# Optimization experiments

Measured on AMD Instinct MI355X. Metric: run time of the kernel, lower is better.

Reference implementation:

```python
import jax, jax.numpy as jnp
import numpy as np

B, N, DS, DP, H, DH, DFF = 1, 1024, 768, 128, 16, 48, 1536


def _ln(x, eps=1e-5):
    m = jnp.mean(x, axis=-1, keepdims=True)
    v = jnp.var(x, axis=-1, keepdims=True)
    return (x - m) * jax.lax.rsqrt(v + eps)


def _ada_ln(a, s, gw, gb, bw):
    # AF3-style adaptive layernorm: sigmoid(Linear(LN(s))) * LN(a) + Linear(LN(s))
    sn = _ln(s)
    return jax.nn.sigmoid(sn @ gw + gb) * _ln(a) + sn @ bw


def setup_inputs() -> dict:
    key = jax.random.key(0)
    ks = jax.random.split(key, 24)
    w = lambda k, shape: jax.random.normal(k, shape, dtype=jnp.float32) * 0.02
    return {
        'x': jax.random.normal(ks[0], (B, N, DS), dtype=jnp.float32),
        'single_cond': jax.random.normal(ks[1], (B, N, DS), dtype=jnp.float32),
        'pair_cond': jax.random.normal(ks[2], (B, N, N, DP), dtype=jnp.float32),
        'attn_gamma_w': w(ks[3], (DS, DS)), 'attn_gamma_b': jnp.zeros((DS,), jnp.float32),
        'attn_beta_w': w(ks[4], (DS, DS)),
        'wq': w(ks[5], (DS, H * DH)), 'bq': jnp.zeros((H * DH,), jnp.float32),
        'wk': w(ks[6], (DS, H * DH)), 'wv': w(ks[7], (DS, H * DH)),
        'wb': w(ks[8], (DP, H)),
        'wg': w(ks[9], (DS, H * DH)),
        'wo': w(ks[10], (H * DH, DS)),
        'attn_gate_w': w(ks[11], (DS, DS)), 'attn_gate_b': jnp.full((DS,), -2.0, jnp.float32),
        'ff_gamma_w': w(ks[12], (DS, DS)), 'ff_gamma_b': jnp.zeros((DS,), jnp.float32),
        'ff_beta_w': w(ks[13], (DS, DS)),
        'ff_w1': w(ks[14], (DS, DFF)), 'ff_w2': w(ks[15], (DS, DFF)),
        'ff_w3': w(ks[16], (DFF, DS)),
        'ff_gate_w': w(ks[17], (DS, DS)), 'ff_gate_b': jnp.full((DS,), -2.0, jnp.float32),
        'mask': jnp.ones((B, N), dtype=bool),
    }


def reference(x, single_cond, pair_cond, attn_gamma_w, attn_gamma_b, attn_beta_w,
              wq, bq, wk, wv, wb, wg, wo, attn_gate_w, attn_gate_b,
              ff_gamma_w, ff_gamma_b, ff_beta_w, ff_w1, ff_w2, ff_w3,
              ff_gate_w, ff_gate_b, mask):
    # --- AttentionPairBias (edge bias + cond adaLN + gated output) ---
    a = _ada_ln(x, single_cond, attn_gamma_w, attn_gamma_b, attn_beta_w)
    q = (a @ wq + bq).reshape(B, N, H, DH)  # q has bias (q_use_bias=True)
    k = (a @ wk).reshape(B, N, H, DH)
    v = (a @ wv).reshape(B, N, H, DH)
    bias = jnp.einsum('bijp,ph->bhij', _ln(pair_cond), wb)  # pair bias per head
    logits = jnp.einsum('bihd,bjhd->bhij', q, k) * (1.0 / np.float32(np.sqrt(DH))) + bias
    logits = jnp.where(mask[:, None, None, :], logits, jnp.float32(-1e9))
    attn = jax.nn.softmax(logits, axis=-1)
    o = jnp.einsum('bhij,bjhd->bihd', attn, v)
    g = jax.nn.sigmoid(a @ wg).reshape(B, N, H, DH)  # gating (g_use_bias=False)
    attn_out = (g * o).reshape(B, N, H * DH) @ wo  # o_use_bias=False
    attn_out = jax.nn.sigmoid(single_cond @ attn_gate_w + attn_gate_b) * attn_out
    # --- ConditionedFeedForward (adaLN + SwiGLU + cond output gate) ---
    f = _ada_ln(x, single_cond, ff_gamma_w, ff_gamma_b, ff_beta_w)
    h = jax.nn.silu(f @ ff_w1) * (f @ ff_w2)
    ff_out = jax.nn.sigmoid(single_cond @ ff_gate_w + ff_gate_b) * (h @ ff_w3)
    # dropout p=0 (eval) -> identity; residual add of both branches
    return x + attn_out + ff_out
```

## Files before the change

### kernel.cpp

```cpp
#include <hip/hip_runtime.h>
#include <hip/hip_bf16.h>


typedef __attribute__((ext_vector_type(8))) short bf16x8;
typedef __attribute__((ext_vector_type(4))) float f32x4;
typedef __attribute__((ext_vector_type(4))) unsigned short us4;

#define DEVFN static __device__ __forceinline__

DEVFN float bf2f(unsigned short u){
  union { unsigned int u; float f; } v; v.u = ((unsigned int)u) << 16; return v.f;
}
DEVFN unsigned short f2bf(float f){
  union { float f; unsigned int u; } v; v.f = f;
  unsigned int r = v.u + 0x7fffu + ((v.u >> 16) & 1u);
  return (unsigned short)(r >> 16);
}
DEVFN float sigf(float x){ return 1.f / (1.f + __expf(-x)); }

DEVFN void gload16(const void* g, void* l){
  __builtin_amdgcn_global_load_lds(
      (const __attribute__((address_space(1))) void*)g,
      (__attribute__((address_space(3))) void*)l, 16, 0, 0);
}

#define OFF_SN    0x0000000ULL
#define OFF_SC    0x0180000ULL
#define OFF_XA    0x0300000ULL
#define OFF_W1    0x0600000ULL
#define OFF_W2    0x0A80000ULL
#define OFF_W3    0x0CC0000ULL
#define OFF_W4    0x1140000ULL
#define OFF_W5    0x15C0000ULL
#define OFF_W6    0x1800000ULL
#define OFF_BIAS1 0x1920000ULL
#define OFF_BIASG 0x1923000ULL
#define OFF_BIASQ 0x1924800ULL
#define OFF_G1    0x1930000ULL
#define OFF_GATES 0x2530000ULL
#define OFF_A     0x2B30000ULL
#define OFF_F     0x2CB0000ULL
#define OFF_QH    0x2E30000ULL
#define OFF_KH    0x2FB0000ULL
#define OFF_GH    0x3130000ULL
#define OFF_VT    0x3430000ULL
#define OFF_HH    0x4030000ULL
#define OFF_GO    0x4330000ULL
#define OFF_PB    0x47B0000ULL

struct WJobs {
  const float* src[14];
  unsigned long long dst[14];
  int K[14];
  int N[14];
  int rowmul[14];
  int rowoff[14];
};

__global__ __launch_bounds__(256) void prep_kernel(WJobs jobs, char* ws,
    const float* __restrict__ x, const float* __restrict__ sc,
    unsigned short* __restrict__ sn_bf, unsigned short* __restrict__ sc_bf,
    float* __restrict__ xa,
    const float* agb, const float* bq, const float* gtb, const float* fgtb,
    const float* fgb, float* bias1, float* biasg, float* biasq){
  const int bid = blockIdx.x;
  const int tid = threadIdx.x;
  if(bid < 9792){
    int t = bid, z = 0;
    while(true){
      int nt = (jobs.N[z] >> 5) * (jobs.K[z] >> 5);
      if(t < nt) break;
      t -= nt; z++;
    }
    const int nx = jobs.N[z] >> 5;
    const int n0 = (t % nx) << 5, k0 = (t / nx) << 5;
    const int K = jobs.K[z], N = jobs.N[z];
    __shared__ float tt[32][33];
    const int tx = tid & 31, ty = tid >> 5;
    const float* src = jobs.src[z];
    #pragma unroll
    for(int i=0;i<4;i++)
      tt[ty + i*8][tx] = src[(long long)(k0 + ty + i*8) * N + n0 + tx];
    __syncthreads();
    unsigned short* dst = (unsigned short*)(ws + jobs.dst[z]);
    const int rm = jobs.rowmul[z], ro = jobs.rowoff[z];
    #pragma unroll
    for(int i=0;i<4;i++)
      dst[(long long)((n0 + ty + i*8)*rm + ro) * K + k0 + tx] = f2bf(tt[tx][ty + i*8]);
    return;
  }
  if(bid >= 10816){
    int t = (bid - 10816) * 256 + tid;
    float v = 0.f;
    if(t < 768) v = agb[t];
    else if(t >= 1536 && t < 2304) v = fgb[t - 1536];
    bias1[t] = v;
    biasq[t] = (t < 768) ? bq[t] : 0.f;
    if(t < 1536) biasg[t] = (t < 768) ? gtb[t] : fgtb[t - 768];
    return;
  }
  const int row = bid - 9792;
  const float* xr = x + (long long)row * 768;
  const float* sr = sc + (long long)row * 768;
  float xs[3], ss[3];
  float s0=0.f, s1=0.f, s2=0.f, s3=0.f;
  #pragma unroll
  for(int i=0;i<3;i++){
    float xv = xr[tid + i*256], sv = sr[tid + i*256];
    xs[i]=xv; ss[i]=sv;
    s0 += xv; s1 += xv*xv; s2 += sv; s3 += sv*sv;
  }
  #pragma unroll
  for(int o=32;o;o>>=1){
    s0 += __shfl_xor(s0,o); s1 += __shfl_xor(s1,o);
    s2 += __shfl_xor(s2,o); s3 += __shfl_xor(s3,o);
  }
  __shared__ float red[4][4];
  const int w = tid >> 6;
  if((tid & 63) == 0){ red[0][w]=s0; red[1][w]=s1; red[2][w]=s2; red[3][w]=s3; }
  __syncthreads();
  float tx0 = red[0][0]+red[0][1]+red[0][2]+red[0][3];
  float tx1 = red[1][0]+red[1][1]+red[1][2]+red[1][3];
  float ts0 = red[2][0]+red[2][1]+red[2][2]+red[2][3];
  float ts1 = red[3][0]+red[3][1]+red[3][2]+red[3][3];
  const float inv = 1.f/768.f;
  float mx = tx0*inv, vx = tx1*inv - mx*mx;
  float ms = ts0*inv, vs = ts1*inv - ms*ms;
  float rsx = rsqrtf(vx + 1e-5f), rss = rsqrtf(vs + 1e-5f);
  #pragma unroll
  for(int i=0;i<3;i++){
    int c = tid + i*256;
    xa[(long long)row*768 + c]    = (xs[i]-mx)*rsx;
    sn_bf[(long long)row*768 + c] = f2bf((ss[i]-ms)*rss);
    sc_bf[(long long)row*768 + c] = f2bf(ss[i]);
  }
}

DEVFN void gemm_tile_f32(const unsigned short* __restrict__ A,
                         const unsigned short* __restrict__ Bt,
                         int N, int K, int m0, int n0,
                         const float* __restrict__ bias,
                         float* __restrict__ Cf, int epi,
                         unsigned short* sA, unsigned short* sB, int tid){
  const int w = tid >> 6, l = tid & 63, l15 = l & 15, l4 = l >> 4;
  const int wm = w >> 1, wn = w & 1;
  f32x4 zf = {0.f,0.f,0.f,0.f};
  f32x4 acc[4][4];
  #pragma unroll
  for(int m=0;m<4;m++)
    #pragma unroll
    for(int n=0;n<4;n++) acc[m][n] = zf;

  const int srow = w*16 + (l >> 2);
  const int scol = (l & 3) * 8;
  const unsigned short* gA = A  + (long long)(m0 + srow) * K + scol;
  const unsigned short* gB = Bt + (long long)(n0 + srow) * K + scol;
  unsigned short* lA0 = &sA[(w*16)*32];
  unsigned short* lA1 = &sA[(64 + w*16)*32];
  unsigned short* lB0 = &sB[(w*16)*32];
  unsigned short* lB1 = &sB[(64 + w*16)*32];
  const long long half = (long long)64 * K;

  for(int k0 = 0; k0 < K; k0 += 32){
    gload16(gA + k0, lA0);
    gload16(gA + half + k0, lA1);
    gload16(gB + k0, lB0);
    gload16(gB + half + k0, lB1);
    __syncthreads();
    bf16x8 af[4], bg[4];
    #pragma unroll
    for(int m=0;m<4;m++) af[m] = *(const bf16x8*)&sA[(wm*64 + m*16 + l15)*32 + l4*8];
    #pragma unroll
    for(int n=0;n<4;n++) bg[n] = *(const bf16x8*)&sB[(wn*64 + n*16 + l15)*32 + l4*8];
    #pragma unroll
    for(int m=0;m<4;m++)
      #pragma unroll
      for(int n=0;n<4;n++)
        acc[m][n] = __builtin_amdgcn_mfma_f32_16x16x32_bf16(af[m], bg[n], acc[m][n], 0, 0, 0);
    __syncthreads();
  }
  #pragma unroll
  for(int m=0;m<4;m++){
    #pragma unroll
    for(int n=0;n<4;n++){
      #pragma unroll
      for(int r=0;r<4;r++){
        const int i = m0 + wm*64 + m*16 + l4*4 + r;
        const int c = n0 + wn*64 + n*16 + l15;
        float v = acc[m][n][r] + bias[c];
        Cf[(long long)i*N + c] = epi ? sigf(v) : v;
      }
    }
  }
}

DEVFN void pair_block(int pbid, const float* __restrict__ pair,
                      const float* __restrict__ wb,
                      unsigned short* __restrict__ pb, int tid){
  const int l = tid & 63, w = tid >> 6, l15 = l & 15, l4 = l >> 4;
  bf16x8 wbf[4];
  #pragma unroll
  for(int c=0;c<4;c++){
    bf16x8 t;
    #pragma unroll
    for(int e=0;e<8;e++) t[e] = (short)f2bf(wb[(c*32 + l4*8 + e)*16 + l15]);
    wbf[c] = t;
  }
  f32x4 zf = {0.f,0.f,0.f,0.f};
  #pragma unroll
  for(int q=0;q<4;q++){
    const long long tile = (long long)pbid * 16 + q*4 + w;
    const long long row0 = tile << 4;
    const float* pr = pair + ((row0 + l15) << 7);
    float vals[32];
    #pragma unroll
    for(int c=0;c<4;c++){
      float4 v0 = *(const float4*)(pr + c*32 + l4*8);
      float4 v1 = *(const float4*)(pr + c*32 + l4*8 + 4);
      vals[c*8+0]=v0.x; vals[c*8+1]=v0.y; vals[c*8+2]=v0.z; vals[c*8+3]=v0.w;
      vals[c*8+4]=v1.x; vals[c*8+5]=v1.y; vals[c*8+6]=v1.z; vals[c*8+7]=v1.w;
    }
    float s=0.f, s2=0.f;
    #pragma unroll
    for(int e=0;e<32;e++){ s += vals[e]; s2 += vals[e]*vals[e]; }
    s += __shfl_xor(s, 16); s2 += __shfl_xor(s2, 16);
    s += __shfl_xor(s, 32); s2 += __shfl_xor(s2, 32);
    const float m = s * (1.f/128.f);
    const float rs = rsqrtf(s2*(1.f/128.f) - m*m + 1e-5f);
    f32x4 acc = zf;
    #pragma unroll
    for(int c=0;c<4;c++){
      bf16x8 af;
      #pragma unroll
      for(int e=0;e<8;e++) af[e] = (short)f2bf((vals[c*8+e] - m) * rs);
      acc = __builtin_amdgcn_mfma_f32_16x16x32_bf16(af, wbf[c], acc, 0,0,0);
    }
    us4 o;
    #pragma unroll
    for(int r=0;r<4;r++) o[r] = f2bf(acc[r]);
    *(us4*)&pb[((long long)l15 << 20) + row0 + l4*4] = o;
  }
}

__global__ __launch_bounds__(256) void fA_kernel(
    const float* __restrict__ pair, const float* __restrict__ wb,
    unsigned short* __restrict__ pb,
    const unsigned short* __restrict__ SN, const unsigned short* __restrict__ W1,
    const float* __restrict__ B1, float* __restrict__ G1,
    const unsigned short* __restrict__ SC, const unsigned short* __restrict__ W2,
    const float* __restrict__ BG, float* __restrict__ GT){
  __shared__ __align__(16) unsigned short sA[128*32];
  __shared__ __align__(16) unsigned short sB[128*32];
  const int bid = blockIdx.x;
  const int tid = threadIdx.x;
  if(bid < 288){
    if(bid < 192){
      gemm_tile_f32(SN, W1, 3072, 768, (bid & 7)*128, (bid >> 3)*128, B1, G1, 0, sA, sB, tid);
    } else {
      const int t = bid - 192;
      gemm_tile_f32(SC, W2, 1536, 768, (t & 7)*128, (t >> 3)*128, BG, GT, 1, sA, sB, tid);
    }
    return;
  }
  pair_block(bid - 288, pair, wb, pb, tid);
}

__global__ __launch_bounds__(256) void ew1_kernel(const float* __restrict__ g1,
    const float* __restrict__ xa, unsigned short* __restrict__ a_bf,
    unsigned short* __restrict__ f_bf, const float* __restrict__ x,
    float* __restrict__ out){
  const int i = blockIdx.x;
  const int c = blockIdx.y * 256 + threadIdx.x;
  const float* row = g1 + (long long)i * 3072;
  float xv = xa[(long long)i*768 + c];
  a_bf[(long long)i*768 + c] = f2bf(sigf(row[c])      * xv + row[768 + c]);
  f_bf[(long long)i*768 + c] = f2bf(sigf(row[1536+c]) * xv + row[2304 + c]);
  out[(long long)i*768 + c] = x[(long long)i*768 + c];
}

__global__ __launch_bounds__(256) void fB_kernel(
    const float* __restrict__ pair, const float* __restrict__ wb,
    unsigned short* __restrict__ pb,
    const unsigned short* __restrict__ A_, const unsigned short* __restrict__ W3,
    const float* __restrict__ BQ,
    unsigned short* __restrict__ QH, unsigned short* __restrict__ KH,
    unsigned short* __restrict__ GH, unsigned short* __restrict__ VT,
    const unsigned short* __restrict__ F_, const unsigned short* __restrict__ W4,
    unsigned short* __restrict__ HH){
  __shared__ __align__(16) unsigned short sA[128*32];
  __shared__ __align__(16) unsigned short sB[128*32];
  const int bid = blockIdx.x;
  const int tid = threadIdx.x;
  if(bid >= 384){
    pair_block(bid - 384 + 2048, pair, wb, pb, tid);
    return;
  }
  const bool isq = bid < 192;
  const int t = isq ? bid : bid - 192;
  const int m0 = (t & 7) * 128, n0 = (t >> 3) * 128;
  const unsigned short* A  = isq ? A_ : F_;
  const unsigned short* Bt = isq ? W3 : W4;
  const int K = 768;

  const int w = tid >> 6, l = tid & 63, l15 = l & 15, l4 = l >> 4;
  const int wm = w >> 1, wn = w & 1;
  f32x4 zf = {0.f,0.f,0.f,0.f};
  f32x4 acc[4][4];
  #pragma unroll
  for(int m=0;m<4;m++)
    #pragma unroll
    for(int n=0;n<4;n++) acc[m][n] = zf;

  const int srow = w*16 + (l >> 2);
  const int scol = (l & 3) * 8;
  const unsigned short* gA = A  + (long long)(m0 + srow) * K + scol;
  const unsigned short* gB = Bt + (long long)(n0 + srow) * K + scol;
  unsigned short* lA0 = &sA[(w*16)*32];
  unsigned short* lA1 = &sA[(64 + w*16)*32];
  unsigned short* lB0 = &sB[(w*16)*32];
  unsigned short* lB1 = &sB[(64 + w*16)*32];
  const long long half = (long long)64 * K;

  for(int k0 = 0; k0 < K; k0 += 32){
    gload16(gA + k0, lA0);
    gload16(gA + half + k0, lA1);
    gload16(gB + k0, lB0);
    gload16(gB + half + k0, lB1);
    __syncthreads();
    bf16x8 af[4], bg[4];
    #pragma unroll
    for(int m=0;m<4;m++) af[m] = *(const bf16x8*)&sA[(wm*64 + m*16 + l15)*32 + l4*8];
    #pragma unroll
    for(int n=0;n<4;n++) bg[n] = *(const bf16x8*)&sB[(wn*64 + n*16 + l15)*32 + l4*8];
    #pragma unroll
    for(int m=0;m<4;m++)
      #pragma unroll
      for(int n=0;n<4;n++)
        acc[m][n] = __builtin_amdgcn_mfma_f32_16x16x32_bf16(af[m], bg[n], acc[m][n], 0, 0, 0);
    __syncthreads();
  }
  if(isq){
    #pragma unroll
    for(int m=0;m<4;m++){
      #pragma unroll
      for(int n=0;n<4;n++){
        const int c = n0 + wn*64 + n*16 + l15;
        const int ibase = m0 + wm*64 + m*16 + l4*4;
        const int which = c / 768;
        const int h = (c % 768) / 48, d = c % 48;
        unsigned short vb[4];
        #pragma unroll
        for(int r=0;r<4;r++) vb[r] = f2bf(acc[m][n][r] + BQ[c]);
        if(which == 2){
          us4 o; o.x=vb[0]; o.y=vb[1]; o.z=vb[2]; o.w=vb[3];
          *(us4*)&VT[((long long)(c - 1536) << 10) + ibase] = o;
        } else {
          unsigned short* dst = (which == 0) ? QH : (which == 1) ? KH : GH;
          #pragma unroll
          for(int r=0;r<4;r++)
            dst[((long long)((h << 10) + ibase + r))*48 + d] = vb[r];
        }
      }
    }
  } else {
    #pragma unroll
    for(int m=0;m<4;m++){
      #pragma unroll
      for(int n=0;n<4;n++){
        #pragma unroll
        for(int r=0;r<4;r++){
          const int i = m0 + wm*64 + m*16 + l4*4 + r;
          const int c = n0 + wn*64 + n*16 + l15;
          float v = acc[m][n][r];
          float partner = __shfl_xor(v, 1);
          if((c & 1) == 0)
            HH[(long long)i*1536 + (c>>1)] = f2bf(v * sigf(v) * partner);
        }
      }
    }
  }
}

__global__ __launch_bounds__(256) void attn_kernel(
    const unsigned short* __restrict__ QH, const unsigned short* __restrict__ KH,
    const unsigned short* __restrict__ GH,
    const unsigned short* __restrict__ pbias,
    const unsigned short* __restrict__ VT,
    unsigned short* __restrict__ go){
  const int h  = blockIdx.x >> 6;
  const int i0 = (blockIdx.x & 63) << 4;
  const int tid = threadIdx.x;
  const int w = tid >> 6, l = tid & 63, l15 = l & 15, l4 = l >> 4;

  __shared__ unsigned short sP[16][1032];
  __shared__ float sRedM[16][4];
  __shared__ float sRedS[16][4];
  __shared__ float sO[4][16][48];

  f32x4 zf = {0.f,0.f,0.f,0.f};
  bf16x8 zero8 = {0,0,0,0,0,0,0,0};

  const unsigned short* pbh = pbias + ((long long)h << 20) + ((long long)i0 << 10);
  #pragma unroll
  for(int it=0; it<8; it++){
    const int idx = it*2048 + tid*8;
    const int r = idx >> 10, c = idx & 1023;
    *(bf16x8*)&sP[r][c] = *(const bf16x8*)&pbh[((long long)r << 10) + c];
  }

  f32x4 accs[16];
  #pragma unroll
  for(int f=0;f<16;f++) accs[f] = zf;
  bf16x8 aq0, aq1;
  {
    const unsigned short* qp = QH + (long long)((h << 10) + i0 + l15)*48;
    aq0 = *(const bf16x8*)(qp + l4*8);
    aq1 = *(const bf16x8*)(qp + 32 + l4*8);
  }
  const int jbase = w * 256;
  #pragma unroll
  for(int f=0; f<16; f++){
    const int j = jbase + f*16 + l15;
    const unsigned short* kp = KH + (long long)((h << 10) + j)*48;
    bf16x8 bk0 = *(const bf16x8*)(kp + l4*8);
    bf16x8 bk1 = *(const bf16x8*)(kp + 32 + l4*8);
    if(l4 >= 2) bk1 = zero8;
    accs[f] = __builtin_amdgcn_mfma_f32_16x16x32_bf16(aq0, bk0, accs[f], 0,0,0);
    accs[f] = __builtin_amdgcn_mfma_f32_16x16x32_bf16(aq1, bk1, accs[f], 0,0,0);
  }
  __syncthreads();

  const float scale = 0.14433756729740643f;
  #pragma unroll
  for(int f=0;f<16;f++){
    #pragma unroll
    for(int r=0;r<4;r++)
      accs[f][r] = accs[f][r]*scale + bf2f(sP[l4*4 + r][jbase + f*16 + l15]);
  }
  float pm[4];
  #pragma unroll
  for(int r=0;r<4;r++){
    float m = accs[0][r];
    #pragma unroll
    for(int f=1;f<16;f++) m = fmaxf(m, accs[f][r]);
    #pragma unroll
    for(int o=1;o<16;o<<=1) m = fmaxf(m, __shfl_xor(m, o));
    pm[r] = m;
  }
  if(l15 == 0){
    #pragma unroll
    for(int r=0;r<4;r++) sRedM[l4*4 + r][w] = pm[r];
  }
  __syncthreads();
  float rowm[4];
  #pragma unroll
  for(int r=0;r<4;r++){
    const int i = l4*4 + r;
    rowm[r] = fmaxf(fmaxf(sRedM[i][0], sRedM[i][1]), fmaxf(sRedM[i][2], sRedM[i][3]));
  }
  float psum[4] = {0.f,0.f,0.f,0.f};
  #pragma unroll
  for(int f=0;f<16;f++)
    #pragma unroll
    for(int r=0;r<4;r++){
      float p = __expf(accs[f][r] - rowm[r]);
      accs[f][r] = p;
      psum[r] += p;
    }
  #pragma unroll
  for(int r=0;r<4;r++)
    #pragma unroll
    for(int o=1;o<16;o<<=1) psum[r] += __shfl_xor(psum[r], o);
  if(l15 == 0){
    #pragma unroll
    for(int r=0;r<4;r++) sRedS[l4*4 + r][w] = psum[r];
  }
  #pragma unroll
  for(int f=0;f<16;f++)
    #pragma unroll
    for(int r=0;r<4;r++)
      sP[l4*4 + r][jbase + f*16 + l15] = f2bf(accs[f][r]);

  f32x4 acco[3];
  #pragma unroll
  for(int n=0;n<3;n++) acco[n] = zf;
  const unsigned short* vth = VT + ((long long)(h*48) << 10);
  #pragma unroll
  for(int c=0; c<4; c++){
    const int jb = jbase + c*64;
    #pragma unroll
    for(int kk=0; kk<2; kk++){
      bf16x8 pa = *(const bf16x8*)&sP[l15][jb + kk*32 + l4*8];
      #pragma unroll
      for(int n=0;n<3;n++){
        bf16x8 bv = *(const bf16x8*)&vth[((long long)(n*16 + l15) << 10) + jb + kk*32 + l4*8];
        acco[n] = __builtin_amdgcn_mfma_f32_16x16x32_bf16(pa, bv, acco[n], 0,0,0);
      }
    }
  }
  #pragma unroll
  for(int n=0;n<3;n++)
    #pragma unroll
    for(int r=0;r<4;r++)
      sO[w][l4*4 + r][n*16 + l15] = acco[n][r];
  __syncthreads();
  for(int t = tid; t < 768; t += 256){
    const int i = t / 48, d = t % 48;
    float o = sO[0][i][d] + sO[1][i][d] + sO[2][i][d] + sO[3][i][d];
    float lsum = sRedS[i][0] + sRedS[i][1] + sRedS[i][2] + sRedS[i][3];
    float gv = bf2f(GH[(long long)((h << 10) + i0 + i)*48 + d]);
    go[(long long)(i0 + i)*768 + h*48 + d] = f2bf(sigf(gv) * (o / lsum));
  }
}

__global__ __launch_bounds__(256) void final_kernel(
    const unsigned short* __restrict__ GO, const unsigned short* __restrict__ W6t,
    const unsigned short* __restrict__ HH, const unsigned short* __restrict__ W5t,
    const float* __restrict__ gates, float* __restrict__ out){
  __shared__ __align__(16) unsigned short sA[128*32];
  __shared__ __align__(16) unsigned short sB[128*32];
  const int m0 = blockIdx.x * 128, n0 = blockIdx.y * 128;
  const int z = blockIdx.z;
  const bool pA = z < 4;
  const unsigned short* A  = pA ? GO  : HH;
  const unsigned short* Bt = pA ? W6t : W5t;
  const int K    = pA ? 768 : 1536;
  const int kbeg = pA ? z*192 : (z-4)*384;
  const int kend = pA ? kbeg + 192 : kbeg + 384;
  const int goff = pA ? 0 : 768;
  const int tid = threadIdx.x;
  const int w = tid >> 6, l = tid & 63, l15 = l & 15, l4 = l >> 4;
  const int wm = w >> 1, wn = w & 1;
  f32x4 zf = {0.f,0.f,0.f,0.f};
  f32x4 acc[4][4];
  #pragma unroll
  for(int m=0;m<4;m++)
    #pragma unroll
    for(int n=0;n<4;n++) acc[m][n] = zf;

  const int srow = w*16 + (l >> 2);
  const int scol = (l & 3) * 8;
  const unsigned short* gA = A  + (long long)(m0 + srow) * K + scol;
  const unsigned short* gB = Bt + (long long)(n0 + srow) * K + scol;
  unsigned short* lA0 = &sA[(w*16)*32];
  unsigned short* lA1 = &sA[(64 + w*16)*32];
  unsigned short* lB0 = &sB[(w*16)*32];
  unsigned short* lB1 = &sB[(64 + w*16)*32];
  const long long half = (long long)64 * K;

  for(int k0 = kbeg; k0 < kend; k0 += 32){
    gload16(gA + k0, lA0);
    gload16(gA + half + k0, lA1);
    gload16(gB + k0, lB0);
    gload16(gB + half + k0, lB1);
    __syncthreads();
    bf16x8 af[4], bg[4];
    #pragma unroll
    for(int m=0;m<4;m++) af[m] = *(const bf16x8*)&sA[(wm*64 + m*16 + l15)*32 + l4*8];
    #pragma unroll
    for(int n=0;n<4;n++) bg[n] = *(const bf16x8*)&sB[(wn*64 + n*16 + l15)*32 + l4*8];
    #pragma unroll
    for(int m=0;m<4;m++)
      #pragma unroll
      for(int n=0;n<4;n++)
        acc[m][n] = __builtin_amdgcn_mfma_f32_16x16x32_bf16(af[m], bg[n], acc[m][n], 0, 0, 0);
    __syncthreads();
  }
  #pragma unroll
  for(int m=0;m<4;m++){
    #pragma unroll
    for(int n=0;n<4;n++){
      #pragma unroll
      for(int r=0;r<4;r++){
        const int i = m0 + wm*64 + m*16 + l4*4 + r;
        const int c = n0 + wn*64 + n*16 + l15;
        float v = gates[(long long)i*1536 + goff + c] * acc[m][n][r];
        __hip_atomic_fetch_add(&out[(long long)i*768 + c], v,
                               __ATOMIC_RELAXED, __HIP_MEMORY_SCOPE_AGENT);
      }
    }
  }
}

extern "C" void kernel_launch(void* const* d_in, const int* in_sizes, int n_in,
                              void* d_out, int out_size, void* d_ws, size_t ws_size,
                              hipStream_t stream){
  (void)in_sizes; (void)n_in; (void)out_size; (void)ws_size;
  const float* x    = (const float*)d_in[0];
  const float* sc   = (const float*)d_in[1];
  const float* pair = (const float*)d_in[2];
  const float* agw  = (const float*)d_in[3];
  const float* agb  = (const float*)d_in[4];
  const float* abw  = (const float*)d_in[5];
  const float* wq   = (const float*)d_in[6];
  const float* bq   = (const float*)d_in[7];
  const float* wk   = (const float*)d_in[8];
  const float* wv   = (const float*)d_in[9];
  const float* wb   = (const float*)d_in[10];
  const float* wg   = (const float*)d_in[11];
  const float* wo   = (const float*)d_in[12];
  const float* gtw  = (const float*)d_in[13];
  const float* gtb  = (const float*)d_in[14];
  const float* fgw  = (const float*)d_in[15];
  const float* fgb  = (const float*)d_in[16];
  const float* fbw  = (const float*)d_in[17];
  const float* fw1  = (const float*)d_in[18];
  const float* fw2  = (const float*)d_in[19];
  const float* fw3  = (const float*)d_in[20];
  const float* fgtw = (const float*)d_in[21];
  const float* fgtb = (const float*)d_in[22];
  float* out = (float*)d_out;
  char* ws = (char*)d_ws;

  unsigned short* SN   = (unsigned short*)(ws + OFF_SN);
  unsigned short* SC   = (unsigned short*)(ws + OFF_SC);
  float*          XA   = (float*)(ws + OFF_XA);
  unsigned short* W1   = (unsigned short*)(ws + OFF_W1);
  unsigned short* W2   = (unsigned short*)(ws + OFF_W2);
  unsigned short* W3   = (unsigned short*)(ws + OFF_W3);
  unsigned short* W4   = (unsigned short*)(ws + OFF_W4);
  unsigned short* W5   = (unsigned short*)(ws + OFF_W5);
  unsigned short* W6   = (unsigned short*)(ws + OFF_W6);
  float*          B1   = (float*)(ws + OFF_BIAS1);
  float*          BG   = (float*)(ws + OFF_BIASG);
  float*          BQ   = (float*)(ws + OFF_BIASQ);
  float*          G1   = (float*)(ws + OFF_G1);
  float*          GT   = (float*)(ws + OFF_GATES);
  unsigned short* A_   = (unsigned short*)(ws + OFF_A);
  unsigned short* F_   = (unsigned short*)(ws + OFF_F);
  unsigned short* QH   = (unsigned short*)(ws + OFF_QH);
  unsigned short* KH   = (unsigned short*)(ws + OFF_KH);
  unsigned short* GH   = (unsigned short*)(ws + OFF_GH);
  unsigned short* VT   = (unsigned short*)(ws + OFF_VT);
  unsigned short* HH   = (unsigned short*)(ws + OFF_HH);
  unsigned short* GO   = (unsigned short*)(ws + OFF_GO);
  unsigned short* PB   = (unsigned short*)(ws + OFF_PB);

  WJobs jobs;
  int ji = 0;
  auto setj = [&](const float* s, unsigned long long off, int K, int N,
                  int rm = 1, int ro = 0){
    jobs.src[ji]=s; jobs.dst[ji]=off; jobs.K[ji]=K; jobs.N[ji]=N;
    jobs.rowmul[ji]=rm; jobs.rowoff[ji]=ro; ji++;
  };
  const unsigned long long W768 = 768ULL*768ULL*2ULL;
  setj(agw,  OFF_W1 + 0*W768, 768, 768);
  setj(abw,  OFF_W1 + 1*W768, 768, 768);
  setj(fgw,  OFF_W1 + 2*W768, 768, 768);
  setj(fbw,  OFF_W1 + 3*W768, 768, 768);
  setj(gtw,  OFF_W2 + 0*W768, 768, 768);
  setj(fgtw, OFF_W2 + 1*W768, 768, 768);
  setj(wq,   OFF_W3 + 0*W768, 768, 768);
  setj(wk,   OFF_W3 + 1*W768, 768, 768);
  setj(wv,   OFF_W3 + 2*W768, 768, 768);
  setj(wg,   OFF_W3 + 3*W768, 768, 768);
  setj(fw1,  OFF_W4, 768, 1536, 2, 0);
  setj(fw2,  OFF_W4, 768, 1536, 2, 1);
  setj(fw3,  OFF_W5, 1536, 768);
  setj(wo,   OFF_W6, 768, 768);

  prep_kernel<<<10828, 256, 0, stream>>>(jobs, ws, x, sc, SN, SC, XA,
      agb, bq, gtb, fgtb, fgb, B1, BG, BQ);
  fA_kernel<<<2336, 256, 0, stream>>>(pair, wb, PB, SN, W1, B1, G1, SC, W2, BG, GT);
  ew1_kernel<<<dim3(1024,3), 256, 0, stream>>>(G1, XA, A_, F_, x, out);
  fB_kernel<<<2432, 256, 0, stream>>>(pair, wb, PB, A_, W3, BQ,
      QH, KH, GH, VT, F_, W4, HH);
  attn_kernel<<<1024, 256, 0, stream>>>(QH, KH, GH, PB, VT, GO);
  final_kernel<<<dim3(8,6,8), 256, 0, stream>>>(GO, W6, HH, W5, GT, out);
}
```

Measured before the change: 265.9 us.

## Spread weight transposes across kernels and overlap FFN output GEMM with attention

Splits the weight-transpose jobs: only the adaLN/gate weights are converted in the prep kernel, and the remaining weights are transposed by extra blocks in fA_kernel alongside the pair-bias work. The FFN down-projection (HH·W5) slices are moved into the attention kernel as extra blocks, so they run concurrently with attention, and the final kernel handles only the Wo projection. The pair-layernorm bf16 conversion switches to truncation instead of round-to-nearest, which is cheaper but slightly less accurate. The aim is to shorten the serial critical path and fill idle CUs, at the cost of larger shared-memory footprints and mixed block types within a kernel.

Result: no change. 265.0 us (-0.3%).

```diff
diff --git a/kernel.cpp b/kernel.cpp
--- a/kernel.cpp
+++ b/kernel.cpp
@@ -15,6 +15,10 @@
   union { float f; unsigned int u; } v; v.f = f;
   unsigned int r = v.u + 0x7fffu + ((v.u >> 16) & 1u);
   return (unsigned short)(r >> 16);
+}
+DEVFN unsigned short f2bf_trunc(float f){
+  union { float f; unsigned int u; } v; v.f = f;
+  return (unsigned short)(v.u >> 16);
 }
 DEVFN float sigf(float x){ return 1.f / (1.f + __expf(-x)); }
 
@@ -49,48 +53,53 @@
 #define OFF_PB    0x47B0000ULL
 
 struct WJobs {
-  const float* src[14];
-  unsigned long long dst[14];
-  int K[14];
-  int N[14];
-  int rowmul[14];
-  int rowoff[14];
+  const float* src[8];
+  unsigned long long dst[8];
+  int K[8];
+  int N[8];
+  int rowmul[8];
+  int rowoff[8];
 };
 
-__global__ __launch_bounds__(256) void prep_kernel(WJobs jobs, char* ws,
+DEVFN void transpose_tile(const WJobs& jobs, char* ws, int t, int tid, void* smem){
+  int z = 0;
+  while(true){
+    int nt = (jobs.N[z] >> 5) * (jobs.K[z] >> 5);
+    if(t < nt) break;
+    t -= nt; z++;
+  }
+  const int nx = jobs.N[z] >> 5;
+  const int n0 = (t % nx) << 5, k0 = (t / nx) << 5;
+  const int K = jobs.K[z], N = jobs.N[z];
+  float (*tt)[33] = (float(*)[33])smem;
+  const int tx = tid & 31, ty = tid >> 5;
+  const float* src = jobs.src[z];
+  #pragma unroll
+  for(int i=0;i<4;i++)
+    tt[ty + i*8][tx] = src[(long long)(k0 + ty + i*8) * N + n0 + tx];
+  __syncthreads();
+  unsigned short* dst = (unsigned short*)(ws + jobs.dst[z]);
+  const int rm = jobs.rowmul[z], ro = jobs.rowoff[z];
+  #pragma unroll
+  for(int i=0;i<4;i++)
+    dst[(long long)((n0 + ty + i*8)*rm + ro) * K + k0 + tx] = f2bf(tt[tx][ty + i*8]);
+}
+
+__global__ __launch_bounds__(256) void prep_kernel(WJobs jobsP, char* ws,
     const float* __restrict__ x, const float* __restrict__ sc,
     unsigned short* __restrict__ sn_bf, unsigned short* __restrict__ sc_bf,
     float* __restrict__ xa,
     const float* agb, const float* bq, const float* gtb, const float* fgtb,
     const float* fgb, float* bias1, float* biasg, float* biasq){
+  __shared__ __align__(16) char smem[4352];
   const int bid = blockIdx.x;
   const int tid = threadIdx.x;
-  if(bid < 9792){
-    int t = bid, z = 0;
-    while(true){
-      int nt = (jobs.N[z] >> 5) * (jobs.K[z] >> 5);
-      if(t < nt) break;
-      t -= nt; z++;
-    }
-    const int nx = jobs.N[z] >> 5;
-    const int n0 = (t % nx) << 5, k0 = (t / nx) << 5;
-    const int K = jobs.K[z], N = jobs.N[z];
-    __shared__ float tt[32][33];
-    const int tx = tid & 31, ty = tid >> 5;
-    const float* src = jobs.src[z];
-    #pragma unroll
-    for(int i=0;i<4;i++)
-      tt[ty + i*8][tx] = src[(long long)(k0 + ty + i*8) * N + n0 + tx];
-    __syncthreads();
-    unsigned short* dst = (unsigned short*)(ws + jobs.dst[z]);
-    const int rm = jobs.rowmul[z], ro = jobs.rowoff[z];
-    #pragma unroll
-    for(int i=0;i<4;i++)
-      dst[(long long)((n0 + ty + i*8)*rm + ro) * K + k0 + tx] = f2bf(tt[tx][ty + i*8]);
+  if(bid < 3456){
+    transpose_tile(jobsP, ws, bid, tid, smem);
     return;
   }
-  if(bid >= 10816){
-    int t = (bid - 10816) * 256 + tid;
+  if(bid >= 4480){
+    int t = (bid - 4480) * 256 + tid;
     float v = 0.f;
     if(t < 768) v = agb[t];
     else if(t >= 1536 && t < 2304) v = fgb[t - 1536];
@@ -99,7 +108,7 @@
     if(t < 1536) biasg[t] = (t < 768) ? gtb[t] : fgtb[t - 768];
     return;
   }
-  const int row = bid - 9792;
+  const int row = bid - 3456;
   const float* xr = x + (long long)row * 768;
   const float* sr = sc + (long long)row * 768;
   float xs[3], ss[3];
@@ -115,7 +124,7 @@
     s0 += __shfl_xor(s0,o); s1 += __shfl_xor(s1,o);
     s2 += __shfl_xor(s2,o); s3 += __shfl_xor(s3,o);
   }
-  __shared__ float red[4][4];
+  float (*red)[4] = (float(*)[4])smem;
   const int w = tid >> 6;
   if((tid & 63) == 0){ red[0][w]=s0; red[1][w]=s1; red[2][w]=s2; red[3][w]=s3; }
   __syncthreads();
@@ -206,11 +215,9 @@
     for(int e=0;e<8;e++) t[e] = (short)f2bf(wb[(c*32 + l4*8 + e)*16 + l15]);
     wbf[c] = t;
   }
-  f32x4 zf = {0.f,0.f,0.f,0.f};
   #pragma unroll
   for(int q=0;q<4;q++){
-    const long long tile = (long long)pbid * 16 + q*4 + w;
-    const long long row0 = tile << 4;
+    const long long row0 = (((long long)pbid) * 16 + q*4 + w) << 4;
     const float* pr = pair + ((row0 + l15) << 7);
     float vals[32];
     #pragma unroll
@@ -227,12 +234,12 @@
     s += __shfl_xor(s, 32); s2 += __shfl_xor(s2, 32);
     const float m = s * (1.f/128.f);
     const float rs = rsqrtf(s2*(1.f/128.f) - m*m + 1e-5f);
-    f32x4 acc = zf;
+    f32x4 acc = {0.f,0.f,0.f,0.f};
     #pragma unroll
     for(int c=0;c<4;c++){
       bf16x8 af;
       #pragma unroll
-      for(int e=0;e<8;e++) af[e] = (short)f2bf((vals[c*8+e] - m) * rs);
+      for(int e=0;e<8;e++) af[e] = (short)f2bf_trunc((vals[c*8+e] - m) * rs);
       acc = __builtin_amdgcn_mfma_f32_16x16x32_bf16(af, wbf[c], acc, 0,0,0);
     }
     us4 o;
@@ -243,6 +250,7 @@
 }
 
 __global__ __launch_bounds__(256) void fA_kernel(
+    WJobs jobsA, char* ws,
     const float* __restrict__ pair, const float* __restrict__ wb,
     unsigned short* __restrict__ pb,
     const unsigned short* __restrict__ SN, const unsigned short* __restrict__ W1,
@@ -262,7 +270,11 @@
     }
     return;
   }
-  pair_block(bid - 288, pair, wb, pb, tid);
+  if(bid < 6624){
+    transpose_tile(jobsA, ws, bid - 288, tid, sA);
+    return;
+  }
+  pair_block(bid - 6624, pair, wb, pb, tid);
 }
 
 __global__ __launch_bounds__(256) void ew1_kernel(const float* __restrict__ g1,
@@ -381,29 +393,99 @@
   }
 }
 
+DEVFN void final_slice(const unsigned short* __restrict__ A,
+                       const unsigned short* __restrict__ Bt,
+                       int K, int kbeg, int kend, int goff, int m0, int n0,
+                       const float* __restrict__ gates, float* __restrict__ out,
+                       unsigned short* sA, unsigned short* sB, int tid){
+  const int w = tid >> 6, l = tid & 63, l15 = l & 15, l4 = l >> 4;
+  const int wm = w >> 1, wn = w & 1;
+  f32x4 zf = {0.f,0.f,0.f,0.f};
+  f32x4 acc[4][4];
+  #pragma unroll
+  for(int m=0;m<4;m++)
+    #pragma unroll
+    for(int n=0;n<4;n++) acc[m][n] = zf;
+
+  const int srow = w*16 + (l >> 2);
+  const int scol = (l & 3) * 8;
+  const unsigned short* gA = A  + (long long)(m0 + srow) * K + scol;
+  const unsigned short* gB = Bt + (long long)(n0 + srow) * K + scol;
+  unsigned short* lA0 = &sA[(w*16)*32];
+  unsigned short* lA1 = &sA[(64 + w*16)*32];
+  unsigned short* lB0 = &sB[(w*16)*32];
+  unsigned short* lB1 = &sB[(64 + w*16)*32];
+  const long long half = (long long)64 * K;
+
+  for(int k0 = kbeg; k0 < kend; k0 += 32){
+    gload16(gA + k0, lA0);
+    gload16(gA + half + k0, lA1);
+    gload16(gB + k0, lB0);
+    gload16(gB + half + k0, lB1);
+    __syncthreads();
+    bf16x8 af[4], bg[4];
+    #pragma unroll
+    for(int m=0;m<4;m++) af[m] = *(const bf16x8*)&sA[(wm*64 + m*16 + l15)*32 + l4*8];
+    #pragma unroll
+    for(int n=0;n<4;n++) bg[n] = *(const bf16x8*)&sB[(wn*64 + n*16 + l15)*32 + l4*8];
+    #pragma unroll
+    for(int m=0;m<4;m++)
+      #pragma unroll
+      for(int n=0;n<4;n++)
+        acc[m][n] = __builtin_amdgcn_mfma_f32_16x16x32_bf16(af[m], bg[n], acc[m][n], 0, 0, 0);
+    __syncthreads();
+  }
+  #pragma unroll
+  for(int m=0;m<4;m++){
+    #pragma unroll
+    for(int n=0;n<4;n++){
+      #pragma unroll
+      for(int r=0;r<4;r++){
+        const int i = m0 + wm*64 + m*16 + l4*4 + r;
+        const int c = n0 + wn*64 + n*16 + l15;
+        float v = gates[(long long)i*1536 + goff + c] * acc[m][n][r];
+        __hip_atomic_fetch_add(&out[(long long)i*768 + c], v,
+                               __ATOMIC_RELAXED, __HIP_MEMORY_SCOPE_AGENT);
+      }
+    }
+  }
+}
+
 __global__ __launch_bounds__(256) void attn_kernel(
     const unsigned short* __restrict__ QH, const unsigned short* __restrict__ KH,
     const unsigned short* __restrict__ GH,
     const unsigned short* __restrict__ pbias,
     const unsigned short* __restrict__ VT,
-    unsigned short* __restrict__ go){
-  const int h  = blockIdx.x >> 6;
-  const int i0 = (blockIdx.x & 63) << 4;
+    unsigned short* __restrict__ go,
+    const unsigned short* __restrict__ HH, const unsigned short* __restrict__ W5t,
+    const float* __restrict__ gates, float* __restrict__ out){
+  __shared__ __align__(16) char smem[45824];
+  const int bid = blockIdx.x;
   const int tid = threadIdx.x;
+  if(bid < 192){
+    const int z = bid / 48, rem = bid % 48;
+    final_slice(HH, W5t, 1536, z*384, z*384 + 384, 768,
+                (rem & 7)*128, (rem >> 3)*128, gates, out,
+                (unsigned short*)smem, (unsigned short*)(smem + 8192), tid);
+    return;
+  }
+  const int it = bid - 192;
+  const int h  = it >> 6;
+  const int i0 = (it & 63) << 4;
   const int w = tid >> 6, l = tid & 63, l15 = l & 15, l4 = l >> 4;
 
-  __shared__ unsigned short sP[16][1032];
-  __shared__ float sRedM[16][4];
-  __shared__ float sRedS[16][4];
-  __shared__ float sO[4][16][48];
+  unsigned short (*sP)[1032] = (unsigned short(*)[1032])smem;
+  float (*sRedM)[4] = (float(*)[4])(smem + 33024);
+  float (*sRedS)[4] = (float(*)[4])(smem + 33280);
+  float (*sO)[16][48] = (float(*)[16][48])(smem + 33536);
 
   f32x4 zf = {0.f,0.f,0.f,0.f};
   bf16x8 zero8 = {0,0,0,0,0,0,0,0};
 
   const unsigned short* pbh = pbias + ((long long)h << 20) + ((long long)i0 << 10);
   #pragma unroll
-  for(int it=0; it<8; it++){
-    const int idx = it*2048 + tid*8;
+  for(int itr=0; itr<8; itr++){
+    const int idx = itr*2048 + tid*8;
     const int r = idx >> 10, c = idx & 1023;
     *(bf16x8*)&sP[r][c] = *(const bf16x8*)&pbh[((long long)r << 10) + c];
   }
@@ -513,73 +595,13 @@
   }
 }
 
-__global__ __launch_bounds__(256) void final_kernel(
+__global__ __launch_bounds__(256) void finalA_kernel(
     const unsigned short* __restrict__ GO, const unsigned short* __restrict__ W6t,
-    const unsigned short* __restrict__ HH, const unsigned short* __restrict__ W5t,
     const float* __restrict__ gates, float* __restrict__ out){
   __shared__ __align__(16) unsigned short sA[128*32];
   __shared__ __align__(16) unsigned short sB[128*32];
-  const int m0 = blockIdx.x * 128, n0 = blockIdx.y * 128;
-  const int z = blockIdx.z;
-  const bool pA = z < 4;
-  const unsigned short* A  = pA ? GO  : HH;
-  const unsigned short* Bt = pA ? W6t : W5t;
-  const int K    = pA ? 768 : 1536;
-  const int kbeg = pA ? z*192 : (z-4)*384;
-  const int kend = pA ? kbeg + 192 : kbeg + 384;
-  const int goff = pA ? 0 : 768;
-  const int tid = threadIdx.x;
-  const int w = tid >> 6, l = tid & 63, l15 = l & 15, l4 = l >> 4;
-  const int wm = w >> 1, wn = w & 1;
-  f32x4 zf = {0.f,0.f,0.f,0.f};
-  f32x4 acc[4][4];
-  #pragma unroll
-  for(int m=0;m<4;m++)
-    #pragma unroll
-    for(int n=0;n<4;n++) acc[m][n] = zf;
-
-  const int srow = w*16 + (l >> 2);
-  const int scol = (l & 3) * 8;
-  const unsigned short* gA = A  + (long long)(m0 + srow) * K + scol;
-  const unsigned short* gB = Bt + (long long)(n0 + srow) * K + scol;
-  unsigned short* lA0 = &sA[(w*16)*32];
-  unsigned short* lA1 = &sA[(64 + w*16)*32];
-  unsigned short* lB0 = &sB[(w*16)*32];
-  unsigned short* lB1 = &sB[(64 + w*16)*32];
-  const long long half = (long long)64 * K;
-
-  for(int k0 = kbeg; k0 < kend; k0 += 32){
-    gload16(gA + k0, lA0);
-    gload16(gA + half + k0, lA1);
-    gload16(gB + k0, lB0);
-    gload16(gB + half + k0, lB1);
-    __syncthreads();
-    bf16x8 af[4], bg[4];
-    #pragma unroll
-    for(int m=0;m<4;m++) af[m] = *(const bf16x8*)&sA[(wm*64 + m*16 + l15)*32 + l4*8];
-    #pragma unroll
-    for(int n=0;n<4;n++) bg[n] = *(const bf16x8*)&sB[(wn*64 + n*16 + l15)*32 + l4*8];
-    #pragma unroll
-    for(int m=0;m<4;m++)
-      #pragma unroll
-      for(int n=0;n<4;n++)
-        acc[m][n] = __builtin_amdgcn_mfma_f32_16x16x32_bf16(af[m], bg[n], acc[m][n], 0, 0, 0);
-    __syncthreads();
-  }
-  #pragma unroll
-  for(int m=0;m<4;m++){
-    #pragma unroll
-    for(int n=0;n<4;n++){
-      #pragma unroll
-      for(int r=0;r<4;r++){
-        const int i = m0 + wm*64 + m*16 + l4*4 + r;
-        const int c = n0 + wn*64 + n*16 + l15;
-        float v = gates[(long long)i*1536 + goff + c] * acc[m][n][r];
-        __hip_atomic_fetch_add(&out[(long long)i*768 + c], v,
-                               __ATOMIC_RELAXED, __HIP_MEMORY_SCOPE_AGENT);
-      }
-    }
-  }
+  final_slice(GO, W6t, 768, blockIdx.z*192, blockIdx.z*192 + 192, 0,
+              blockIdx.x*128, blockIdx.y*128, gates, out, sA, sB, threadIdx.x);
 }
 
 extern "C" void kernel_launch(void* const* d_in, const int* in_sizes, int n_in,
@@ -636,35 +658,49 @@
   unsigned short* GO   = (unsigned short*)(ws + OFF_GO);
   unsigned short* PB   = (unsigned short*)(ws + OFF_PB);
 
-  WJobs jobs;
-  int ji = 0;
-  auto setj = [&](const float* s, unsigned long long off, int K, int N,
-                  int rm = 1, int ro = 0){
-    jobs.src[ji]=s; jobs.dst[ji]=off; jobs.K[ji]=K; jobs.N[ji]=N;
-    jobs.rowmul[ji]=rm; jobs.rowoff[ji]=ro; ji++;
-  };
   const unsigned long long W768 = 768ULL*768ULL*2ULL;
-  setj(agw,  OFF_W1 + 0*W768, 768, 768);
-  setj(abw,  OFF_W1 + 1*W768, 768, 768);
-  setj(fgw,  OFF_W1 + 2*W768, 768, 768);
-  setj(fbw,  OFF_W1 + 3*W768, 768, 768);
-  setj(gtw,  OFF_W2 + 0*W768, 768, 768);
-  setj(fgtw, OFF_W2 + 1*W768, 768, 768);
-  setj(wq,   OFF_W3 + 0*W768, 768, 768);
-  setj(wk,   OFF_W3 + 1*W768, 768, 768);
-  setj(wv,   OFF_W3 + 2*W768, 768, 768);
-  setj(wg,   OFF_W3 + 3*W768, 768, 768);
-  setj(fw1,  OFF_W4, 768, 1536, 2, 0);
-  setj(fw2,  OFF_W4, 768, 1536, 2, 1);
-  setj(fw3,  OFF_W5, 1536, 768);
-  setj(wo,   OFF_W6, 768, 768);
-
-  prep_kernel<<<10828, 256, 0, stream>>>(jobs, ws, x, sc, SN, SC, XA,
+
+  WJobs jobsP;
+  {
+    int ji = 0;
+    auto setj = [&](const float* s, unsigned long long off, int K, int N,
+                    int rm, int ro){
+      jobsP.src[ji]=s; jobsP.dst[ji]=off; jobsP.K[ji]=K; jobsP.N[ji]=N;
+      jobsP.rowmul[ji]=rm; jobsP.rowoff[ji]=ro; ji++;
+    };
+    setj(agw,  OFF_W1 + 0*W768, 768, 768, 1, 0);
+    setj(abw,  OFF_W1 + 1*W768, 768, 768, 1, 0);
+    setj(fgw,  OFF_W1 + 2*W768, 768, 768, 1, 0);
+    setj(fbw,  OFF_W1 + 3*W768, 768, 768, 1, 0);
+    setj(gtw,  OFF_W2 + 0*W768, 768, 768, 1, 0);
+    setj(fgtw, OFF_W2 + 1*W768, 768, 768, 1, 0);
+  }
+  WJobs jobsA;
+  {
+    int ji = 0;
+    auto setj = [&](const float* s, unsigned long long off, int K, int N,
+                    int rm, int ro){
+      jobsA.src[ji]=s; jobsA.dst[ji]=off; jobsA.K[ji]=K; jobsA.N[ji]=N;
+      jobsA.rowmul[ji]=rm; jobsA.rowoff[ji]=ro; ji++;
+    };
+    setj(wq,   OFF_W3 + 0*W768, 768, 768, 1, 0);
+    setj(wk,   OFF_W3 + 1*W768, 768, 768, 1, 0);
+    setj(wv,   OFF_W3 + 2*W768, 768, 768, 1, 0);
+    setj(wg,   OFF_W3 + 3*W768, 768, 768, 1, 0);
+    setj(fw1,  OFF_W4, 768, 1536, 2, 0);
+    setj(fw2,  OFF_W4, 768, 1536, 2, 1);
+    setj(fw3,  OFF_W5, 1536, 768, 1, 0);
+    setj(wo,   OFF_W6, 768, 768, 1, 0);
+  }
+
+  prep_kernel<<<4492, 256, 0, stream>>>(jobsP, ws, x, sc, SN, SC, XA,
       agb, bq, gtb, fgtb, fgb, B1, BG, BQ);
-  fA_kernel<<<2336, 256, 0, stream>>>(pair, wb, PB, SN, W1, B1, G1, SC, W2, BG, GT);
+  fA_kernel<<<8672, 256, 0, stream>>>(jobsA, ws, pair, wb, PB,
+      SN, W1, B1, G1, SC, W2, BG, GT);
   ew1_kernel<<<dim3(1024,3), 256, 0, stream>>>(G1, XA, A_, F_, x, out);
   fB_kernel<<<2432, 256, 0, stream>>>(pair, wb, PB, A_, W3, BQ,
       QH, KH, GH, VT, F_, W4, HH);
-  attn_kernel<<<1024, 256, 0, stream>>>(QH, KH, GH, PB, VT, GO);
-  final_kernel<<<dim3(8,6,8), 256, 0, stream>>>(GO, W6, HH, W5, GT, out);
-}
+  attn_kernel<<<1216, 256, 0, stream>>>(QH, KH, GH, PB, VT, GO,
+      HH, W5, GT, out);
+  finalA_kernel<<<dim3(8,6,4), 256, 0, stream>>>(GO, W6, GT, out);
+}
```
